# Performance work log

Hardware: AMD Instinct MI355X
Metric: run time of the kernel (lower is better)

Reference implementation:

```python
import jax, jax.numpy as jnp
import numpy as np

B, H, W, DIM = 4, 128, 128, 64
HEADS, DH, DR = 8, 64, 16
INNER = HEADS * DH  # 512
HID3 = 3 * DR       # 48, wavelet-MLP in_channels
HIDX = 2 * HID3     # 96, wavelet-MLP hidden


def _conv(x, w, stride=1, pad=0, groups=1):
    return jax.lax.conv_general_dilated(
        x, w, (stride, stride), [(pad, pad), (pad, pad)],
        dimension_numbers=('NCHW', 'OIHW', 'NCHW'), feature_group_count=groups)


def _gelu(x):
    return jax.nn.gelu(x, approximate=False)  # torch nn.GELU default (erf)


def _haar_kernel(C):
    h = np.array([[1., 1.], [1., 1.]]) / 2.
    g = np.array([[1., -1.], [1., -1.]]) / 2.
    ht = np.array([[1., 1.], [-1., -1.]]) / 2.
    gt = np.array([[1., -1.], [-1., 1.]]) / 2.
    k = np.stack([h, g, ht, gt])[:, None]          # [4,1,2,2]
    return jnp.asarray(np.tile(k, (C, 1, 1, 1)), jnp.float32)  # [4C,1,2,2], torch repeat layout


def _l2norm(x):
    return x / jnp.maximum(jnp.linalg.norm(x, axis=-1, keepdims=True), 1e-12)


def _spatial(x, dw, pw, gamma):  # SpitialUnit, x NHWC
    t = x.transpose(0, 3, 1, 2)
    C = t.shape[1]
    y = _conv(t, dw, pad=1, groups=C)
    y = _conv(_gelu(y), pw)
    return (t + gamma * y).transpose(0, 2, 3, 1)


def _fourier(x, al_pw, al_dw, ah_pw, ah_dw, ph_pw, ph_scale):  # FourierUnit, x NHWC
    t = x.transpose(0, 3, 1, 2)
    Bc, C, Hc, Wc = t.shape
    X = jnp.fft.rfft2(t, norm='ortho')
    amp, phase = jnp.abs(X), jnp.angle(X)
    Hf, Wf = amp.shape[-2], amp.shape[-1]
    yy = jnp.linspace(0., 1., Hf)[:, None]
    xx = jnp.linspace(0., 1., Wf)[None, :]
    rr = jnp.sqrt(yy ** 2 + xx ** 2)
    low = jax.nn.sigmoid((0.25 - rr) * 20.0)
    high = 1.0 - low
    a_lo = _conv(_gelu(_conv(amp * low[None, None], al_pw)), al_dw, pad=1, groups=C)
    a_hi = _conv(_gelu(_conv(amp * high[None, None], ah_pw)), ah_dw, pad=1, groups=C)
    amp_out = a_lo + a_hi
    phase_out = phase + ph_scale * _conv(phase, ph_pw)
    Y = jax.lax.complex(amp_out * jnp.cos(phase_out), amp_out * jnp.sin(phase_out))
    out = jnp.fft.irfft2(Y, s=(Hc, Wc), norm='ortho')
    return out.transpose(0, 2, 3, 1)


def _wavelet(x, bn_gamma, bn_beta, mlp_in, mlp_dw, mlp_out, res_scale):  # WaveletUnit, x NHWC (H,W even)
    t = x.transpose(0, 3, 1, 2)
    Bc, C, Hc, Wc = t.shape
    y = _conv(t, _haar_kernel(C), stride=2, groups=C)           # [B,4C,H/2,W/2]
    LL, LH, HL, HH = jnp.split(y, 4, axis=1)                    # torch chunk layout
    high = jnp.concatenate([LH, HL, HH], axis=1)                # [B,3C,H/2,W/2]
    # BatchNorm2d in eval mode: running_mean=0, running_var=1, eps=1e-5
    n = high * (bn_gamma / jnp.sqrt(1.0 + 1e-5))[None, :, None, None] + bn_beta[None, :, None, None]
    m = _conv(n, mlp_in)
    m = _gelu(_conv(m, mlp_dw, pad=1, groups=m.shape[1]))
    m = _conv(m, mlp_out)
    high_enh = high + res_scale * m
    x1, x2, x3 = jnp.split(high_enh, 3, axis=1)
    # IWT: out[..., 2i+p, 2j+q] = [LL, x1; x2, x3][p,q]
    arr = jnp.stack([jnp.stack([LL, x1], -1), jnp.stack([x2, x3], -1)], axis=-2)  # [B,C,h,w,p,q]
    Hh, Wh = LL.shape[-2], LL.shape[-1]
    out = arr.transpose(0, 1, 2, 4, 3, 5).reshape(Bc, C, Hh * 2, Wh * 2)
    return out.transpose(0, 2, 3, 1)


def reference(x_in, Wq, Wk, Wv, Wr, We, qs_dw, qs_pw, qs_gamma,
              al_pw, al_dw, ah_pw, ah_dw, ph_pw, ph_scale,
              bn_gamma, bn_beta, mlp_in, mlp_dw, mlp_out, res_scale,
              rescale, Wproj, bproj):
    b, h, w, c = x_in.shape
    hw = h * w
    heads = rescale.shape[0]
    dh = Wq.shape[1] // heads
    dr = Wr.shape[1]
    x = x_in.reshape(b, hw, c)
    q_inp, k_inp, v_inp = x @ Wq, x @ Wk, x @ Wv
    q_dim = (q_inp @ Wr).reshape(b, h, w, dr)
    k_dim = (k_inp @ Wr).reshape(b, h, w, dr)
    v_dim = (v_inp @ Wr).reshape(b, h, w, dr)
    q_mix = _spatial(q_dim, qs_dw, qs_pw, qs_gamma)
    k_mix = _fourier(k_dim, al_pw, al_dw, ah_pw, ah_dw, ph_pw, ph_scale)
    v_mix = _wavelet(v_dim, bn_gamma, bn_beta, mlp_in, mlp_dw, mlp_out, res_scale)
    q_new = q_mix.reshape(b, hw, dr) @ We
    k_new = k_mix.reshape(b, hw, dr) @ We
    v_new = v_mix.reshape(b, hw, dr) @ We

    def pack(t):  # -> [b, heads, dh, hw]
        return t.reshape(b, hw, heads, dh).transpose(0, 2, 3, 1)

    q, k, v = pack(q_new), pack(k_new), pack(v_new)
    q, k = _l2norm(q), _l2norm(k)                       # normalize over hw
    attn = jnp.einsum('bhdn,bhen->bhde', k, q)          # channel attention [b,H,dh,dh]
    attn = jax.nn.softmax(attn * rescale[None], axis=-1)
    o = jnp.einsum('bhde,bhen->bhdn', attn, v)          # [b,H,dh,hw]
    o = o.transpose(0, 3, 1, 2).reshape(b, hw, heads * dh)
    return (o @ Wproj + bproj).reshape(b, h, w, c)


def setup_inputs() -> dict:
    key = jax.random.key(0)
    ks = jax.random.split(key, 20)

    def nrm(k, shape, s=0.02):
        return jax.random.normal(k, shape, jnp.float32) * s

    return {
        'x_in': jax.random.normal(ks[0], (B, H, W, DIM), jnp.float32),
        'Wq': nrm(ks[1], (DIM, INNER)), 'Wk': nrm(ks[2], (DIM, INNER)), 'Wv': nrm(ks[3], (DIM, INNER)),
        'Wr': nrm(ks[4], (INNER, DR)), 'We': nrm(ks[5], (DR, INNER)),
        'qs_dw': nrm(ks[6], (DR, 1, 3, 3)), 'qs_pw': nrm(ks[7], (DR, DR, 1, 1)),
        'qs_gamma': jnp.zeros((1, DR, 1, 1), jnp.float32),
        'al_pw': nrm(ks[8], (DR, DR, 1, 1)), 'al_dw': nrm(ks[9], (DR, 1, 3, 3)),
        'ah_pw': nrm(ks[10], (DR, DR, 1, 1)), 'ah_dw': nrm(ks[11], (DR, 1, 3, 3)),
        'ph_pw': nrm(ks[12], (DR, DR, 1, 1)), 'ph_scale': jnp.asarray(0.01, jnp.float32),
        'bn_gamma': jnp.ones((HID3,), jnp.float32), 'bn_beta': jnp.zeros((HID3,), jnp.float32),
        'mlp_in': nrm(ks[13], (HIDX, HID3, 1, 1)), 'mlp_dw': nrm(ks[14], (HIDX, 1, 3, 3)),
        'mlp_out': nrm(ks[15], (HID3, HIDX, 1, 1)), 'res_scale': jnp.ones((1,), jnp.float32),
        'rescale': jnp.ones((HEADS, 1, 1), jnp.float32),
        'Wproj': nrm(ks[16], (INNER, DIM)), 'bproj': jnp.zeros((DIM,), jnp.float32),
    }
```

## Files before the change

kernel.cpp:

```cpp
#include <hip/hip_runtime.h>
#include <hip/hip_bf16.h>
#include <math.h>

#define HW 16384

__device__ __forceinline__ float LD(const void* p, long i, int bf){
  return bf ? __bfloat162float(((const __hip_bfloat16*)p)[i]) : ((const float*)p)[i];
}
__device__ __forceinline__ float geluf(float x){ return 0.5f*x*(1.0f + erff(x*0.70710678118654752f)); }
__device__ __forceinline__ int rev7(int i){ return (int)(__brev((unsigned)i)>>25); }

__device__ __forceinline__ void fft128(float* Ar, float* Ai, const float* ct, const float* st,
                                       int lane, float dir){
  #pragma unroll
  for(int len=2; len<=128; len<<=1){
    int half=len>>1;
    int pos = lane & (half-1);
    int i1 = ((lane & ~(half-1))<<1) | pos;
    int i2 = i1 + half;
    int tw = pos * (128/len);
    float wr = ct[tw], wi = dir*st[tw];
    float xr=Ar[i2], xi=Ai[i2];
    float tr = xr*wr - xi*wi;
    float ti = xr*wi + xi*wr;
    float ur=Ar[i1], ui=Ai[i1];
    Ar[i1]=ur+tr; Ai[i1]=ui+ti;
    Ar[i2]=ur-tr; Ai[i2]=ui-ti;
  }
}

#define MAKE_TWP(ct,st) { int tt=threadIdx.x; if(tt<128){ float ang=6.283185307179586f*(float)tt/128.f; float s_,c_; sincosf(ang,&s_,&c_); (ct)[tt]=c_; (st)[tt]=s_; } }

#define OFF_M    0
#define OFF_G    3072
#define OFF_MB   6144
#define OFF_FLAG 10240
#define OFF_QDIM 16384
#define OFF_KDIM (16384 + 1048576)
#define OFF_VDIM (16384 + 2*1048576)
#define OFF_QMIX (16384 + 3*1048576)
#define OFF_KMIX (16384 + 4*1048576)
#define OFF_S    (16384 + 5*1048576)
#define FSZ 532480

__device__ __forceinline__ void wave_dw_body(int o, const float* m96, float* g96, const float* wdw){
  int ch = o%96; int r = o/96; int px = r&4095; int b = r>>12;
  int i = px>>6, j = px&63;
  long mb = (long)b*393216;
  float acc=0.f;
  for(int dp=0;dp<3;dp++){ int ii=i-1+dp; if(ii<0||ii>=64) continue;
    for(int dq=0;dq<3;dq++){ int jj=j-1+dq; if(jj<0||jj>=64) continue;
      acc += wdw[ch*9+dp*3+dq]*m96[mb + (long)(ii*64+jj)*96 + ch]; } }
  g96[o]=geluf(acc);
}

__global__ void k_head(const void* Wq, const void* Wk, const void* Wv,
                       const void* Wr, const void* bng, float* ws){
  __shared__ float wr[8192];
  __shared__ float part[256];
  int blk=blockIdx.x, t=threadIdx.x;
  if(blk==48){
    for(int i=3072+t;i<10240;i+=256) ws[i]=0.f;
    if(t==0){
      float v = ((const float*)bng)[0];
      ((int*)ws)[OFF_FLAG] = (v==1.0f) ? 0 : 1;
    }
    return;
  }
  int bf = (((const float*)bng)[0]==1.0f) ? 0 : 1;
  int mat=blk>>4, seg=blk&15;
  const void* Wsrc = mat==0 ? Wq : (mat==1 ? Wk : Wv);
  for(int i=t;i<8192;i+=256) wr[i]=LD(Wr,i,bf);
  __syncthreads();
  int o=t&63, jseg=t>>6;
  int c=seg*4+(o>>4), r=o&15;
  float acc=0.f;
  for(int j=jseg*128;j<jseg*128+128;j++) acc += LD(Wsrc,(long)c*512+j,bf)*wr[j*16+r];
  part[jseg*64+o]=acc;
  __syncthreads();
  if(t<64){
    float s=part[t]+part[64+t]+part[128+t]+part[192+t];
    int cc=seg*4+(t>>4), rr=t&15;
    ws[cc*48 + mat*16 + rr]=s;
  }
}

__global__ void k_dims(const void* x, const float* ws,
                       float* qd, float* kd, float* vd, const int* flg){
  int bf=*flg;
  __shared__ __align__(16) float ms[3072];
  __shared__ __align__(16) float xs[64*130];
  int t=threadIdx.x;
  int b = blockIdx.x>>7;
  int pix0 = (blockIdx.x&127)<<7;
  for(int i=t;i<3072;i+=256) ms[i]=ws[i];
  long base = ((long)b*HW + pix0)*64;
  if(!bf){
    const float4* xp = (const float4*)((const float*)x + base);
    for(int e=t;e<2048;e+=256){
      int px=e>>4, c4=(e&15)<<2;
      float4 v = xp[e];
      xs[(c4  )*130+px]=v.x; xs[(c4+1)*130+px]=v.y;
      xs[(c4+2)*130+px]=v.z; xs[(c4+3)*130+px]=v.w;
    }
  } else {
    const uint4* xp = (const uint4*)((const __hip_bfloat16*)x + base);
    for(int e=t;e<1024;e+=256){
      int px=e>>3, c8=(e&7)<<3;
      uint4 u = xp[e];
      unsigned uu[4]={u.x,u.y,u.z,u.w};
      #pragma unroll
      for(int q=0;q<4;q++){
        xs[(c8+2*q  )*130+px] = __uint_as_float((uu[q]&0xffffu)<<16);
        xs[(c8+2*q+1)*130+px] = __uint_as_float(uu[q]&0xffff0000u);
      }
    }
  }
  __syncthreads();
  int pxg=t>>2, rg=t&3;
  int px0=pxg<<1, r0=rg*12;
  float acc0[12], acc1[12];
  #pragma unroll
  for(int j=0;j<12;j++){ acc0[j]=0.f; acc1[j]=0.f; }
  #pragma unroll 4
  for(int c=0;c<64;c++){
    float2 xv = *(const float2*)&xs[c*130+px0];
    const float4* mp = (const float4*)&ms[c*48+r0];
    float4 m0=mp[0], m1=mp[1], m2=mp[2];
    acc0[0]+=xv.x*m0.x; acc0[1]+=xv.x*m0.y; acc0[2]+=xv.x*m0.z; acc0[3]+=xv.x*m0.w;
    acc0[4]+=xv.x*m1.x; acc0[5]+=xv.x*m1.y; acc0[6]+=xv.x*m1.z; acc0[7]+=xv.x*m1.w;
    acc0[8]+=xv.x*m2.x; acc0[9]+=xv.x*m2.y; acc0[10]+=xv.x*m2.z; acc0[11]+=xv.x*m2.w;
    acc1[0]+=xv.y*m0.x; acc1[1]+=xv.y*m0.y; acc1[2]+=xv.y*m0.z; acc1[3]+=xv.y*m0.w;
    acc1[4]+=xv.y*m1.x; acc1[5]+=xv.y*m1.y; acc1[6]+=xv.y*m1.z; acc1[7]+=xv.y*m1.w;
    acc1[8]+=xv.y*m2.x; acc1[9]+=xv.y*m2.y; acc1[10]+=xv.y*m2.z; acc1[11]+=xv.y*m2.w;
  }
  __syncthreads();
  float* sh = xs;
  #pragma unroll
  for(int j=0;j<12;j++){
    sh[(px0  )*49 + r0+j] = acc0[j];
    sh[(px0+1)*49 + r0+j] = acc1[j];
  }
  __syncthreads();
  long ob = ((long)b*HW + pix0)*16;
  for(int e=t;e<2048;e+=256){
    int px=e>>4, rr=e&15;
    qd[ob+e]=sh[px*49 + rr];
    kd[ob+e]=sh[px*49 + 16 + rr];
    vd[ob+e]=sh[px*49 + 32 + rr];
  }
}

__global__ void k_mix3(const float* qd, float* qm, const void* dw, const void* pw, const void* gamma,
                       const float* kd, float* Rre, float* Rim,
                       const float* vd, float* m96, const void* win, const void* bng, const void* bnb,
                       const int* flg){
  __shared__ __align__(16) float smem[9664];
  int bf=*flg;
  int blk=blockIdx.x, t=threadIdx.x;
  if(blk<256){
    float* tile=smem;
    float* dws=smem+9216;
    float* pws=smem+9360;
    float* gsm=smem+9616;
    int b=blk>>6, y0=(blk&63)<<1;
    for(int i=t;i<144;i+=256){ int tap=i>>4, ch=i&15; dws[i]=LD(dw,ch*9+tap,bf); }
    if(t<256) pws[t]=LD(pw,t,bf);
    if(t<16) gsm[t]=LD(gamma,t,bf);
    for(int i=t;i<8192;i+=256){
      int ry=i>>11, rem=i&2047, xx=rem>>4, ch=rem&15;
      int yy=y0-1+ry;
      tile[(ry*128+xx)*18+ch] = (yy>=0&&yy<128) ? qd[(long)(b*128+yy)*2048 + rem] : 0.f;
    }
    __syncthreads();
    int ty=t>>7, x=t&127;
    float2 g2[8];
    #pragma unroll
    for(int k=0;k<8;k++){ g2[k].x=0.f; g2[k].y=0.f; }
    for(int p=0;p<3;p++){
      int row=ty+p;
      for(int q=0;q<3;q++){
        int xx=x-1+q;
        if(xx<0||xx>=128) continue;
        const float2* tv=(const float2*)&tile[(row*128+xx)*18];
        const float2* wv=(const float2*)&dws[(p*3+q)*16];
        #pragma unroll
        for(int k=0;k<8;k++){
          float2 tt=tv[k], ww=wv[k];
          g2[k].x += ww.x*tt.x; g2[k].y += ww.y*tt.y;
        }
      }
    }
    float ge[16];
    #pragma unroll
    for(int k=0;k<8;k++){ ge[2*k]=geluf(g2[k].x); ge[2*k+1]=geluf(g2[k].y); }
    long ob = ((long)(b*128+y0+ty)*128 + x)*16;
    for(int c=0;c<16;c++){
      const float2* pv=(const float2*)&pws[c*16];
      float acc=0.f;
      #pragma unroll
      for(int k=0;k<8;k++){ float2 pp=pv[k]; acc += pp.x*ge[2*k]+pp.y*ge[2*k+1]; }
      qm[ob+c] = tile[((1+ty)*128+x)*18+c] + gsm[c]*acc;
    }
  } else if(blk<512){
    float* slab=smem; float* outre=smem+4160; float* outim=smem+6272;
    float* Ar=smem+8384; float* Ai=smem+8896; float* ct=smem+9408; float* st=smem+9536;
    int blk2=blk-256;
    int b=blk2>>6, y0=(blk2&63)<<1;
    MAKE_TWP(ct,st);
    long gbase = ((long)(b*128+y0))*2048;
    for(int e=t;e<4096;e+=256){
      int yl=e>>11, rem=e&2047, x=rem>>4, c=rem&15;
      slab[yl*2080 + c*130 + x] = kd[gbase + e];
    }
    __syncthreads();
    int w=t>>6, l=t&63, wb=w<<7;
    for(int li=w; li<32; li+=4){
      int yl=li>>4, c=li&15;
      int sb = yl*2080 + c*130;
      float v0=slab[sb+l], v1=slab[sb+64+l];
      int r0=rev7(l), r1=rev7(64+l);
      Ar[wb+r0]=v0; Ai[wb+r0]=0.f;
      Ar[wb+r1]=v1; Ai[wb+r1]=0.f;
      fft128(Ar+wb, Ai+wb, ct, st, l, -1.f);
      int ob = yl*1056 + c*66;
      outre[ob+l]=Ar[wb+l]; outim[ob+l]=Ai[wb+l];
      if(l==0){ outre[ob+64]=Ar[wb+64]; outim[ob+64]=Ai[wb+64]; }
    }
    __syncthreads();
    long obase = ((long)(b*128+y0))*1040;
    for(int e=t;e<2080;e+=256){
      int yl=e/1040, rem=e%1040, v=rem>>4, c=rem&15;
      Rre[obase+e]=outre[yl*1056 + c*66 + v];
      Rim[obase+e]=outim[yl*1056 + c*66 + v];
    }
  } else {
    float* wiT=smem;
    float* vds=smem+4800;
    float* ns =smem+6848;
    float* gsm=smem+8416;
    float* bsm=smem+8464;
    int blk3=blk-512;
    int b = blk3>>7;
    int hpbase = (blk3&127)<<5;
    int i0 = hpbase>>6, j0 = hpbase&63;
    for(int i=t;i<4608;i+=256){ int ch=i/48, cc=i-ch*48; wiT[cc*100+ch]=LD(win,i,bf); }
    if(t<48){ gsm[t]=LD(bng,t,bf)*(1.f/sqrtf(1.f+1e-5f)); bsm[t]=LD(bnb,t,bf); }
    long rb0 = ((long)(b*128 + 2*i0)*128 + 2*j0)*16;
    {
      const float4* v4a=(const float4*)(vd+rb0);
      const float4* v4b=(const float4*)(vd+rb0+2048);
      ((float4*)vds)[t] = v4a[t];
      ((float4*)(vds+1024))[t] = v4b[t];
    }
    __syncthreads();
    for(int o=t;o<1536;o+=256){
      int p=o/48, cc=o-p*48;
      int m=cc+16, c=m>>2, f=m&3;
      float a =vds[(2*p)*16+c],      bv=vds[(2*p+1)*16+c];
      float cv=vds[1024+(2*p)*16+c], dvv=vds[1024+(2*p+1)*16+c];
      float v;
      if(f==0)      v=(a+bv+cv+dvv);
      else if(f==1) v=(a-bv+cv-dvv);
      else if(f==2) v=(a+bv-cv-dvv);
      else          v=(a-bv-cv+dvv);
      ns[p*49+cc] = v*0.5f*gsm[cc]+bsm[cc];
    }
    __syncthreads();
    int px=t>>3, chg=t&7;
    int ch0=chg*12;
    float4 a0={0,0,0,0}, a1={0,0,0,0}, a2={0,0,0,0};
    #pragma unroll 4
    for(int cc=0;cc<48;cc++){
      float nsv = ns[px*49+cc];
      const float4* wp = (const float4*)&wiT[cc*100+ch0];
      float4 w0=wp[0], w1=wp[1], w2=wp[2];
      a0.x+=nsv*w0.x; a0.y+=nsv*w0.y; a0.z+=nsv*w0.z; a0.w+=nsv*w0.w;
      a1.x+=nsv*w1.x; a1.y+=nsv*w1.y; a1.z+=nsv*w1.z; a1.w+=nsv*w1.w;
      a2.x+=nsv*w2.x; a2.y+=nsv*w2.y; a2.z+=nsv*w2.z; a2.w+=nsv*w2.w;
    }
    long ob = ((long)b*4096 + hpbase + px)*96 + ch0;
    float4* mp=(float4*)(m96+ob);
    mp[0]=a0; mp[1]=a1; mp[2]=a2;
  }
}

__global__ void k_fft_col(const float* Rre, const float* Rim,
                          float* glo, float* ghi, float* pho,
                          const void* alpw, const void* ahpw,
                          const void* phpw, const void* phs,
                          const float* m96, float* g96, const void* wdw_,
                          const int* flg){
  __shared__ float sre[2080], sim[2080];
  __shared__ float og[2080], oh[2080], op[2080];
  __shared__ float Ar[512], Ai[512];
  __shared__ float ct[128], st[128];
  __shared__ float wl[256], wh[256], wp[256];
  int t=threadIdx.x;
  int bf=*flg;
  int blk=blockIdx.x;
  if(blk>=260){
    float* wdw=sre;
    for(int i=t;i<864;i+=256) wdw[i]=LD(wdw_,i,bf);
    __syncthreads();
    wave_dw_body((blk-260)*256+t, m96, g96, wdw);
    return;
  }
  int b = blk/65, v = blk%65;
  MAKE_TWP(ct,st);
  wl[t]=LD(alpw,t,bf); wh[t]=LD(ahpw,t,bf); wp[t]=LD(phpw,t,bf);
  long ibase = ((long)b*128)*1040 + v*16;
  for(int e=t;e<2048;e+=256){
    int y=e>>4, c=e&15;
    sre[c*130+y]=Rre[ibase + (long)y*1040 + c];
    sim[c*130+y]=Rim[ibase + (long)y*1040 + c];
  }
  __syncthreads();
  int w=t>>6, l=t&63, wb=w<<7;
  const float inv=1.f/128.f;
  for(int c=w; c<16; c+=4){
    int sb=c*130;
    float x0r=sre[sb+l], x0i=sim[sb+l], x1r=sre[sb+64+l], x1i=sim[sb+64+l];
    int r0=rev7(l), r1=rev7(64+l);
    Ar[wb+r0]=x0r; Ai[wb+r0]=x0i;
    Ar[wb+r1]=x1r; Ai[wb+r1]=x1i;
    fft128(Ar+wb, Ai+wb, ct, st, l, -1.f);
    float re0=Ar[wb+l]*inv, im0=Ai[wb+l]*inv;
    float re1=Ar[wb+64+l]*inv, im1=Ai[wb+64+l]*inv;
    sre[sb+l]=sqrtf(re0*re0+im0*im0); sim[sb+l]=atan2f(im0,re0);
    sre[sb+64+l]=sqrtf(re1*re1+im1*im1); sim[sb+64+l]=atan2f(im1,re1);
  }
  __syncthreads();
  {
    int u = t&127, half = t>>7;
    float yy=(float)u/127.f, xx=(float)v/64.f;
    float rr=sqrtf(yy*yy+xx*xx);
    float lo = 1.f/(1.f+expf((rr-0.25f)*20.f));
    float hi = 1.f-lo;
    float av[16], pv[16];
    for(int ch=0;ch<16;ch++){ av[ch]=sre[ch*130+u]; pv[ch]=sim[ch*130+u]; }
    float pscale = LD(phs,0,bf);
    for(int c=half*8;c<half*8+8;c++){
      float al=0.f, ah=0.f, pp=0.f;
      for(int ch=0;ch<16;ch++){
        float a=av[ch];
        al += wl[c*16+ch]*(a*lo);
        ah += wh[c*16+ch]*(a*hi);
        pp += wp[c*16+ch]*pv[ch];
      }
      og[c*130+u]=geluf(al); oh[c*130+u]=geluf(ah); op[c*130+u]=pv[c]+pscale*pp;
    }
  }
  __syncthreads();
  long obase = ((long)b*128)*1040 + v*16;
  for(int e=t;e<2048;e+=256){
    int u=e>>4, c=e&15;
    long o = obase + (long)u*1040 + c;
    glo[o]=og[c*130+u]; ghi[o]=oh[c*130+u]; pho[o]=op[c*130+u];
  }
}

__global__ void k_four_dw(const float* glo, const float* ghi, const float* pho,
                          float* Yre, float* Yim,
                          const void* aldw, const void* ahdw, const int* flg){
  int bf=*flg;
  __shared__ float wl[144], wh[144];
  int t=threadIdx.x;
  if(t<144){wl[t]=LD(aldw,t,bf); wh[t]=LD(ahdw,t,bf);}
  __syncthreads();
  long o = (long)blockIdx.x*256+t;
  int c=(int)(o&15); long r=o>>4; int v=(int)(r%65); long r2=r/65; int u=(int)(r2&127); int b=(int)(r2>>7);
  float acc=0.f;
  for(int dp=0;dp<3;dp++){
    int uu=u-1+dp; if(uu<0||uu>=128) continue;
    for(int dq=0;dq<3;dq++){
      int vv=v-1+dq; if(vv<0||vv>=65) continue;
      long idx=(((long)(b*128+uu))*65+vv)*16+c;
      acc += wl[c*9+dp*3+dq]*glo[idx] + wh[c*9+dp*3+dq]*ghi[idx];
    }
  }
  float pvv = pho[o];
  float s_,c_; sincosf(pvv,&s_,&c_);
  Yre[o]=acc*c_; Yim[o]=acc*s_;
}

__global__ void k_ifft_col(const float* Yre, const float* Yim, float* Zre, float* Zim,
                           const float* m96, float* g96, const void* wdw_, const int* flg){
  __shared__ float sre[2080], sim[2080];
  __shared__ float Ar[512], Ai[512];
  __shared__ float ct[128], st[128];
  int t=threadIdx.x;
  int blk=blockIdx.x;
  if(blk>=260){
    int bf=*flg;
    float* wdw=sre;
    for(int i=t;i<864;i+=256) wdw[i]=LD(wdw_,i,bf);
    __syncthreads();
    wave_dw_body((blk-260+2048)*256+t, m96, g96, wdw);
    return;
  }
  int b = blk/65, v = blk%65;
  MAKE_TWP(ct,st);
  long ibase = ((long)b*128)*1040 + v*16;
  for(int e=t;e<2048;e+=256){
    int u=e>>4, c=e&15;
    sre[c*130+u]=Yre[ibase + (long)u*1040 + c];
    sim[c*130+u]=Yim[ibase + (long)u*1040 + c];
  }
  __syncthreads();
  int w=t>>6, l=t&63, wb=w<<7;
  for(int c=w; c<16; c+=4){
    int sb=c*130;
    float x0r=sre[sb+l], x0i=sim[sb+l], x1r=sre[sb+64+l], x1i=sim[sb+64+l];
    int r0=rev7(l), r1=rev7(64+l);
    Ar[wb+r0]=x0r; Ai[wb+r0]=x0i;
    Ar[wb+r1]=x1r; Ai[wb+r1]=x1i;
    fft128(Ar+wb, Ai+wb, ct, st, l, +1.f);
    sre[sb+l]=Ar[wb+l]; sim[sb+l]=Ai[wb+l];
    sre[sb+64+l]=Ar[wb+64+l]; sim[sb+64+l]=Ai[wb+64+l];
  }
  __syncthreads();
  for(int e=t;e<2048;e+=256){
    int y=e>>4, c=e&15;
    Zre[ibase + (long)y*1040 + c]=sre[c*130+y];
    Zim[ibase + (long)y*1040 + c]=sim[c*130+y];
  }
}

__global__ void k_irow_gram(const float* Zre, const float* Zim, const float* qm,
                            float* G, const float* m96, float* g96, const void* wdw_,
                            const int* flg){
  __shared__ float smem[9664];
  int blk=blockIdx.x, t=threadIdx.x;
  if(blk>=256){
    int bf=*flg;
    float* wdw=smem;
    for(int i=t;i<864;i+=256) wdw[i]=LD(wdw_,i,bf);
    __syncthreads();
    wave_dw_body((blk-256+4096)*256+t, m96, g96, wdw);
    return;
  }
  float* szre=smem; float* szim=smem+2112; float* oslab=smem+4224;
  float* Ar=smem+8384; float* Ai=smem+8896; float* ct=smem+9408; float* st=smem+9536;
  int b = blk>>6, y0 = (blk&63)<<1;
  MAKE_TWP(ct,st);
  long ibase = ((long)(b*128+y0))*1040;
  for(int e=t;e<2080;e+=256){
    int yl=e/1040, rem=e%1040, v=rem>>4, c=rem&15;
    szre[yl*1056 + c*66 + v]=Zre[ibase+e];
    szim[yl*1056 + c*66 + v]=Zim[ibase+e];
  }
  __syncthreads();
  int w=t>>6, l=t&63, wb=w<<7;
  const float inv=1.f/128.f;
  for(int li=w; li<32; li+=4){
    int yl=li>>4, c=li&15;
    int sb = yl*1056 + c*66;
    float zr0 = szre[sb+l];
    float zi0 = (l==0)?0.f:szim[sb+l];
    float zr1, zi1;
    if(l==0){ zr1=szre[sb+64]; zi1=0.f; }
    else    { zr1=szre[sb+64-l]; zi1=-szim[sb+64-l]; }
    int r0=rev7(l), r1=rev7(64+l);
    Ar[wb+r0]=zr0; Ai[wb+r0]=zi0;
    Ar[wb+r1]=zr1; Ai[wb+r1]=zi1;
    fft128(Ar+wb, Ai+wb, ct, st, l, +1.f);
    int ob = yl*2080 + c*130;
    oslab[ob+l]=Ar[wb+l]*inv;
    oslab[ob+64+l]=Ar[wb+64+l]*inv;
  }
  __syncthreads();
  float* qs = smem;
  long qbase = ((long)(b*128+y0))*2048;
  for(int e=t;e<4096;e+=256) qs[e]=qm[qbase+e];
  __syncthreads();
  int r=t>>4, s=t&15;
  float akq=0.f, akk=0.f, aqq=0.f;
  for(int p=0;p<256;p++){
    int yl=p>>7, x=p&127;
    float kr = oslab[yl*2080 + r*130 + x];
    float ks_ = oslab[yl*2080 + s*130 + x];
    float qr = qs[p*16+r];
    float qsv= qs[p*16+s];
    akq += kr*qsv;
    akk += kr*ks_;
    aqq += qr*qsv;
  }
  float* Gb=G + b*768;
  atomicAdd(&Gb[t], akq);
  atomicAdd(&Gb[256+t], akk);
  atomicAdd(&Gb[512+t], aqq);
}

__global__ void k_attn(const float* G, float* Mb, const void* We,
                       const void* Wproj, const void* resc, const int* flg){
  int bf=*flg;
  __shared__ float wes[16*64];
  __shared__ float gkq[256], gkk[256], gqq[256];
  __shared__ float ukq[64*16], ukk[64*16], uqq[64*16];
  __shared__ float nk[64], nq[64];
  __shared__ float A[64*64];
  __shared__ float T[64*16];
  __shared__ float wpj[64*64];
  int b=blockIdx.x>>3, h=blockIdx.x&7;
  int t=threadIdx.x;
  for(int i=t;i<1024;i+=256){ int rr=i>>6, e=i&63; wes[rr*64+e]=LD(We, (long)rr*512 + h*64 + e, bf); }
  gkq[t]=G[b*768+t]; gkk[t]=G[b*768+256+t]; gqq[t]=G[b*768+512+t];
  for(int i=t;i<4096;i+=256){ int d=i>>6, c=i&63; wpj[i]=LD(Wproj,(long)(h*64+d)*64+c,bf); }
  __syncthreads();
  for(int i=t;i<1024;i+=256){
    int d=i>>4, s=i&15;
    float a1=0.f,a2=0.f,a3=0.f;
    for(int rr=0;rr<16;rr++){ float wv=wes[rr*64+d]; a1+=wv*gkq[rr*16+s]; a2+=wv*gkk[rr*16+s]; a3+=wv*gqq[rr*16+s]; }
    ukq[i]=a1; ukk[i]=a2; uqq[i]=a3;
  }
  __syncthreads();
  if(t<64){ float a=0.f; for(int s=0;s<16;s++) a+=ukk[t*16+s]*wes[s*64+t]; nk[t]=fmaxf(sqrtf(a),1e-12f); }
  else if(t<128){ int e=t-64; float a=0.f; for(int s=0;s<16;s++) a+=uqq[e*16+s]*wes[s*64+e]; nq[e]=fmaxf(sqrtf(a),1e-12f); }
  __syncthreads();
  float rsc=LD(resc,h,bf);
  for(int i=t;i<4096;i+=256){
    int d=i>>6, e=i&63;
    float a=0.f; for(int s=0;s<16;s++) a+=ukq[d*16+s]*wes[s*64+e];
    A[i]=a/(nk[d]*nq[e])*rsc;
  }
  __syncthreads();
  if(t<64){
    int d=t; float m=-1e30f;
    for(int e=0;e<64;e++) m=fmaxf(m,A[d*64+e]);
    float sum=0.f;
    for(int e=0;e<64;e++){ float ev=expf(A[d*64+e]-m); A[d*64+e]=ev; sum+=ev; }
    float inv=1.f/sum;
    for(int e=0;e<64;e++) A[d*64+e]*=inv;
  }
  __syncthreads();
  for(int i=t;i<1024;i+=256){
    int d=i>>4, s=i&15;
    float a=0.f; for(int e=0;e<64;e++) a+=A[d*64+e]*wes[s*64+e];
    T[i]=a;
  }
  __syncthreads();
  for(int i=t;i<1024;i+=256){
    int s=i>>6, c=i&63;
    float a=0.f; for(int d=0;d<64;d++) a+=T[d*16+s]*wpj[d*64+c];
    atomicAdd(&Mb[b*1024 + s*64 + c], a);
  }
}

__global__ void k_epi2(const float* g96, const float* vd, const float* Mb_,
                       const void* wout_, const void* rs_, const void* bproj,
                       void* out, const int* flg){
  int bf=*flg;
  __shared__ __align__(16) float sg[16*104];
  __shared__ __align__(16) float swt[48*100];
  __shared__ __align__(16) float smb[1024];
  __shared__ float sbias[64];
  int t=threadIdx.x;
  int b = blockIdx.x>>8;
  int rem = blockIdx.x&255;
  int gi = rem>>2;
  int gj0 = (rem&3)<<4;

  long gb = ((long)b*4096 + gi*64 + gj0)*96;
  for(int e=t;e<1536;e+=256){ int px=e/96, ch=e-px*96; sg[px*104+ch]=g96[gb+e]; }
  for(int e=t;e<4608;e+=256){ int cc=e/96, ch=e-cc*96; swt[cc*100+ch]=LD(wout_, e, bf); }
  for(int i=t;i<1024;i+=256) smb[i]=Mb_[b*1024+i];
  if(t<64) sbias[t]=LD(bproj,t,bf);
  __syncthreads();

  int px=t>>4, ccg=t&15;
  int cc0=ccg*3;
  float a0=0.f,a1=0.f,a2=0.f;
  const float4* g4=(const float4*)sg;
  const float4* w4=(const float4*)swt;
  #pragma unroll 4
  for(int ch4=0; ch4<24; ch4++){
    float4 ga=g4[px*26+ch4];
    float4 w0=w4[cc0*25+ch4], w1=w4[(cc0+1)*25+ch4], w2=w4[(cc0+2)*25+ch4];
    a0 += ga.x*w0.x+ga.y*w0.y+ga.z*w0.z+ga.w*w0.w;
    a1 += ga.x*w1.x+ga.y*w1.y+ga.z*w1.z+ga.w*w1.w;
    a2 += ga.x*w2.x+ga.y*w2.y+ga.z*w2.z+ga.w*w2.w;
  }
  __syncthreads();

  float* she = sg;
  float rs=LD(rs_,0,bf);
  float accv[3]={a0,a1,a2};
  int gj=gj0+px;
  long vb=((long)(b*128+2*gi)*128 + 2*gj)*16;
  #pragma unroll
  for(int j=0;j<3;j++){
    int cc=cc0+j;
    int m=cc+16, c=m>>2, f=m&3;
    float a=vd[vb+c], bv=vd[vb+16+c], cv=vd[vb+2048+c], dv=vd[vb+2064+c];
    float hv;
    if(f==0)      hv=(a+bv+cv+dv);
    else if(f==1) hv=(a-bv+cv-dv);
    else if(f==2) hv=(a+bv-cv-dv);
    else          hv=(a-bv-cv+dv);
    she[px*64 + 16 + cc] = hv*0.5f + rs*accv[j];
  }
  {
    int c16=ccg;
    int c=c16>>2, f=c16&3;
    float a=vd[vb+c], bv=vd[vb+16+c], cv=vd[vb+2048+c], dv=vd[vb+2064+c];
    float hv;
    if(f==0)      hv=(a+bv+cv+dv);
    else if(f==1) hv=(a-bv+cv-dv);
    else if(f==2) hv=(a+bv-cv-dv);
    else          hv=(a-bv-cv+dv);
    she[px*64 + c16] = hv*0.5f;
  }
  __syncthreads();

  int c=t&63, xg=t>>6;
  float mbr[16];
  #pragma unroll
  for(int s=0;s<16;s++) mbr[s]=smb[s*64+c];
  float bb=sbias[c];
  long ob0 = ((long)(b*128+2*gi)*128 + 2*gj0)*64;
  for(int k=0;k<16;k++){
    int o=xg+(k<<2);
    int r=o>>5, xl=o&31;
    int hp=xl>>1, pos=((r&1)<<1)|(xl&1);
    const float4* h4=(const float4*)(she + hp*64 + pos*16);
    float4 h0=h4[0],h1=h4[1],h2=h4[2],h3=h4[3];
    float acc=bb;
    acc += h0.x*mbr[0]+h0.y*mbr[1]+h0.z*mbr[2]+h0.w*mbr[3];
    acc += h1.x*mbr[4]+h1.y*mbr[5]+h1.z*mbr[6]+h1.w*mbr[7];
    acc += h2.x*mbr[8]+h2.y*mbr[9]+h2.z*mbr[10]+h2.w*mbr[11];
    acc += h3.x*mbr[12]+h3.y*mbr[13]+h3.z*mbr[14]+h3.w*mbr[15];
    long oo = ob0 + (long)r*8192 + (long)xl*64 + c;
    if(bf) ((__hip_bfloat16*)out)[oo]=__float2bfloat16(acc);
    else   ((float*)out)[oo]=acc;
  }
}

extern "C" void kernel_launch(void* const* d_in, const int* in_sizes, int n_in,
                              void* d_out, int out_size, void* d_ws, size_t ws_size,
                              hipStream_t stream) {
  const void* x_in   = d_in[0];
  const void* Wq     = d_in[1];
  const void* Wk     = d_in[2];
  const void* Wv     = d_in[3];
  const void* Wr     = d_in[4];
  const void* We     = d_in[5];
  const void* qs_dw  = d_in[6];
  const void* qs_pw  = d_in[7];
  const void* qs_g   = d_in[8];
  const void* al_pw  = d_in[9];
  const void* al_dw  = d_in[10];
  const void* ah_pw  = d_in[11];
  const void* ah_dw  = d_in[12];
  const void* ph_pw  = d_in[13];
  const void* ph_s   = d_in[14];
  const void* bn_g   = d_in[15];
  const void* bn_b   = d_in[16];
  const void* mlp_in = d_in[17];
  const void* mlp_dw = d_in[18];
  const void* mlp_out= d_in[19];
  const void* res_s  = d_in[20];
  const void* rescale= d_in[21];
  const void* Wproj  = d_in[22];
  const void* bproj  = d_in[23];
  float* ws = (float*)d_ws;
  const int* flg = ((const int*)ws) + OFF_FLAG;

  float* FA = ws + OFF_S;
  float* FB = FA + FSZ;
  float* FC = FB + FSZ;
  float* FD = FC + FSZ;
  float* FE = FD + FSZ;
  float* M96 = FE + FSZ;
  float* G96 = ws + OFF_QDIM;

  k_head<<<49,256,0,stream>>>(Wq,Wk,Wv,Wr,bn_g, ws);
  k_dims<<<512,256,0,stream>>>(x_in, ws, ws+OFF_QDIM, ws+OFF_KDIM, ws+OFF_VDIM, flg);
  k_mix3<<<1024,256,0,stream>>>(ws+OFF_QDIM, ws+OFF_QMIX, qs_dw, qs_pw, qs_g,
                                ws+OFF_KDIM, FA, FB,
                                ws+OFF_VDIM, M96, mlp_in, bn_g, bn_b, flg);
  k_fft_col<<<2308,256,0,stream>>>(FA, FB, FC, FD, FE, al_pw, ah_pw, ph_pw, ph_s,
                                   M96, G96, mlp_dw, flg);
  k_four_dw<<<2080,256,0,stream>>>(FC, FD, FE, FA, FB, al_dw, ah_dw, flg);
  k_ifft_col<<<2308,256,0,stream>>>(FA, FB, FC, FD, M96, G96, mlp_dw, flg);
  k_irow_gram<<<2304,256,0,stream>>>(FC, FD, ws+OFF_QMIX, ws+OFF_G, M96, G96, mlp_dw, flg);
  k_attn<<<32,256,0,stream>>>(ws+OFF_G, ws+OFF_MB, We, Wproj, rescale, flg);
  k_epi2<<<1024,256,0,stream>>>(G96, ws+OFF_VDIM, ws+OFF_MB, mlp_out, res_s, bproj, d_out, flg);
}
```

Measured before the change: 267.6 us.

## Fuse Fourier depthwise conv and phase rotation into inverse column FFT kernel

Removes the separate k_four_dw kernel and computes the 3x3 depthwise amplitude conv plus the sincos phase recombination directly while loading each column into shared memory in the inverse column FFT. This avoids writing and re-reading the Yre/Yim intermediate buffers and saves one kernel launch. The buffer assignments are rotated so the later row-FFT/Gram kernel reads FA/FB. The attention softmax is also parallelised to four threads per row, using shuffles instead of one thread per row. The trade-off is that each block now gathers 3x3 neighbourhoods with strided global reads.

Result: no change. 271.9 us (+1.6%).

```diff
diff --git a/kernel.cpp b/kernel.cpp
--- a/kernel.cpp
+++ b/kernel.cpp
@@ -360,39 +360,19 @@
   }
 }
 
-__global__ void k_four_dw(const float* glo, const float* ghi, const float* pho,
-                          float* Yre, float* Yim,
-                          const void* aldw, const void* ahdw, const int* flg){
-  int bf=*flg;
-  __shared__ float wl[144], wh[144];
-  int t=threadIdx.x;
-  if(t<144){wl[t]=LD(aldw,t,bf); wh[t]=LD(ahdw,t,bf);}
-  __syncthreads();
-  long o = (long)blockIdx.x*256+t;
-  int c=(int)(o&15); long r=o>>4; int v=(int)(r%65); long r2=r/65; int u=(int)(r2&127); int b=(int)(r2>>7);
-  float acc=0.f;
-  for(int dp=0;dp<3;dp++){
-    int uu=u-1+dp; if(uu<0||uu>=128) continue;
-    for(int dq=0;dq<3;dq++){
-      int vv=v-1+dq; if(vv<0||vv>=65) continue;
-      long idx=(((long)(b*128+uu))*65+vv)*16+c;
-      acc += wl[c*9+dp*3+dq]*glo[idx] + wh[c*9+dp*3+dq]*ghi[idx];
-    }
-  }
-  float pvv = pho[o];
-  float s_,c_; sincosf(pvv,&s_,&c_);
-  Yre[o]=acc*c_; Yim[o]=acc*s_;
-}
-
-__global__ void k_ifft_col(const float* Yre, const float* Yim, float* Zre, float* Zim,
-                           const float* m96, float* g96, const void* wdw_, const int* flg){
+__global__ void k_ifft_four(const float* glo, const float* ghi, const float* pho,
+                            float* Zre, float* Zim,
+                            const void* aldw, const void* ahdw,
+                            const float* m96, float* g96, const void* wdw_,
+                            const int* flg){
   __shared__ float sre[2080], sim[2080];
   __shared__ float Ar[512], Ai[512];
   __shared__ float ct[128], st[128];
+  __shared__ float wl[144], wh[144];
   int t=threadIdx.x;
   int blk=blockIdx.x;
+  int bf=*flg;
   if(blk>=260){
-    int bf=*flg;
     float* wdw=sre;
     for(int i=t;i<864;i+=256) wdw[i]=LD(wdw_,i,bf);
     __syncthreads();
@@ -401,11 +381,22 @@
   }
   int b = blk/65, v = blk%65;
   MAKE_TWP(ct,st);
-  long ibase = ((long)b*128)*1040 + v*16;
+  if(t<144){ wl[t]=LD(aldw,t,bf); wh[t]=LD(ahdw,t,bf); }
+  __syncthreads();
   for(int e=t;e<2048;e+=256){
     int u=e>>4, c=e&15;
-    sre[c*130+u]=Yre[ibase + (long)u*1040 + c];
-    sim[c*130+u]=Yim[ibase + (long)u*1040 + c];
+    float acc=0.f;
+    for(int dp=0;dp<3;dp++){
+      int uu=u-1+dp; if(uu<0||uu>=128) continue;
+      for(int dq=0;dq<3;dq++){
+        int vv=v-1+dq; if(vv<0||vv>=65) continue;
+        long idx=(((long)(b*128+uu))*65+vv)*16+c;
+        acc += wl[c*9+dp*3+dq]*glo[idx] + wh[c*9+dp*3+dq]*ghi[idx];
+      }
+    }
+    long o=(((long)(b*128+u))*65+v)*16+c;
+    float s_,c_; sincosf(pho[o],&s_,&c_);
+    sre[c*130+u]=acc*c_; sim[c*130+u]=acc*s_;
   }
   __syncthreads();
   int w=t>>6, l=t&63, wb=w<<7;
@@ -420,6 +411,7 @@
     sre[sb+64+l]=Ar[wb+64+l]; sim[sb+64+l]=Ai[wb+64+l];
   }
   __syncthreads();
+  long ibase = ((long)b*128)*1040 + v*16;
   for(int e=t;e<2048;e+=256){
     int y=e>>4, c=e&15;
     Zre[ibase + (long)y*1040 + c]=sre[c*130+y];
@@ -525,13 +517,18 @@
     A[i]=a/(nk[d]*nq[e])*rsc;
   }
   __syncthreads();
-  if(t<64){
-    int d=t; float m=-1e30f;
-    for(int e=0;e<64;e++) m=fmaxf(m,A[d*64+e]);
+  {
+    int d=t>>2, g=t&3, e0=g<<4;
+    float m=-1e30f;
+    for(int e=e0;e<e0+16;e++) m=fmaxf(m,A[d*64+e]);
+    m=fmaxf(m,__shfl_xor(m,1,4));
+    m=fmaxf(m,__shfl_xor(m,2,4));
     float sum=0.f;
-    for(int e=0;e<64;e++){ float ev=expf(A[d*64+e]-m); A[d*64+e]=ev; sum+=ev; }
+    for(int e=e0;e<e0+16;e++){ float ev=expf(A[d*64+e]-m); A[d*64+e]=ev; sum+=ev; }
+    sum+=__shfl_xor(sum,1,4);
+    sum+=__shfl_xor(sum,2,4);
     float inv=1.f/sum;
-    for(int e=0;e<64;e++) A[d*64+e]*=inv;
+    for(int e=e0;e<e0+16;e++) A[d*64+e]*=inv;
   }
   __syncthreads();
   for(int i=t;i<1024;i+=256){
@@ -681,9 +678,9 @@
                                 ws+OFF_VDIM, M96, mlp_in, bn_g, bn_b, flg);
   k_fft_col<<<2308,256,0,stream>>>(FA, FB, FC, FD, FE, al_pw, ah_pw, ph_pw, ph_s,
                                    M96, G96, mlp_dw, flg);
-  k_four_dw<<<2080,256,0,stream>>>(FC, FD, FE, FA, FB, al_dw, ah_dw, flg);
-  k_ifft_col<<<2308,256,0,stream>>>(FA, FB, FC, FD, M96, G96, mlp_dw, flg);
-  k_irow_gram<<<2304,256,0,stream>>>(FC, FD, ws+OFF_QMIX, ws+OFF_G, M96, G96, mlp_dw, flg);
+  k_ifft_four<<<2308,256,0,stream>>>(FC, FD, FE, FA, FB, al_dw, ah_dw,
+                                     M96, G96, mlp_dw, flg);
+  k_irow_gram<<<2304,256,0,stream>>>(FA, FB, ws+OFF_QMIX, ws+OFF_G, M96, G96, mlp_dw, flg);
   k_attn<<<32,256,0,stream>>>(ws+OFF_G, ws+OFF_MB, We, Wproj, rescale, flg);
   k_epi2<<<1024,256,0,stream>>>(G96, ws+OFF_VDIM, ws+OFF_MB, mlp_out, res_s, bproj, d_out, flg);
 }
```
